# Kernel optimization log

Measured on AMD Instinct MI355X. Metric: run time of the kernel, lower is better.

## Reference

```python
import itertools
import jax, jax.numpy as jnp
import numpy as np


def _lin(x, w, b):
    # LogitsInference with logic_hidden_dim=[] is a single Linear (logits).
    return jnp.einsum('...i,oi->...o', x, w) + b


def _permute_cat(x, order):
    # Permutation(order): concat over all permutations of the `order` variable axes.
    if order <= 1:
        return x
    nd = x.ndim  # [B, n x order, C]
    return jnp.concatenate(
        [jnp.transpose(x, (0,) + p + (nd - 1,))
         for p in itertools.permutations(range(1, order + 1))], axis=-1)


def _expand(x, i, n):
    # Expander(i-1): insert a new object axis at position i (after existing var axes).
    x = jnp.expand_dims(x, axis=i)
    shape = list(x.shape)
    shape[i] = n
    return jnp.broadcast_to(x, tuple(shape))


def _reduce(x, order_in):
    # Reducer(order_in, exclude_self=True): mask entries with repeated indices among
    # the order_in variable axes, then take exists(max)/forall(min) over the last
    # variable axis and interleave channels -> 2*C.
    n = x.shape[1]
    if order_in >= 2:
        idx = [jnp.arange(n).reshape((1,) * k + (n,) + (1,) * (order_in - k - 1))
               for k in range(order_in)]
        mask = jnp.ones((n,) * order_in, dtype=bool)
        for a in range(order_in):
            for b in range(a + 1, order_in):
                mask = mask & (idx[a] != idx[b])
        mask = mask[None, ..., None]  # [1, n x order_in, 1]
        inp0 = jnp.where(mask, x, jnp.zeros((), x.dtype))
        inp1 = jnp.where(mask, x, jnp.ones((), x.dtype))
    else:
        inp0 = inp1 = x
    exists = jnp.max(inp0, axis=-2)
    forall = jnp.min(inp1, axis=-2)
    out = jnp.stack([exists, forall], axis=-1)  # interleave like torch stack+view
    return out.reshape(out.shape[:-2] + (out.shape[-2] * 2,))


def _bmask(act, bit, ndim):
    return act[:, bit].astype(jnp.float32).reshape((-1,) + (1,) * (ndim - 1))


def _logic_layer(x0, x1, x2, x3,
                 w_op0, b_op0, w_red0, b_red0,
                 w_exp1, b_exp1, w_op1, b_op1, w_red1, b_red1,
                 w_exp2, b_exp2, w_op2, b_op2, w_red2, b_red2,
                 w_exp3, b_exp3, w_op3, b_op3, act):
    n = x1.shape[1]
    # Per-batch-item bit masks replace index_select/index_copy_ (same math:
    # selected rows get the branch output, others contribute zero to the sum).
    # order 0: bits 0 (direct), 1 (reduce from order 1)
    s0 = (_bmask(act, 0, 2) * _lin(x0, w_op0, b_op0)
          + _bmask(act, 1, 2) * _lin(_reduce(x1, 1), w_red0, b_red0))
    o0 = jnp.where(jnp.any(act[:, 0:2] == 1), jax.nn.sigmoid(s0), jnp.zeros_like(s0))
    # order 1: bits 2 (expand from 0), 3 (direct), 4 (reduce from 2)
    s1 = (_bmask(act, 2, 3) * _lin(_expand(x0, 1, n), w_exp1, b_exp1)
          + _bmask(act, 3, 3) * _lin(x1, w_op1, b_op1)
          + _bmask(act, 4, 3) * _lin(_reduce(x2, 2), w_red1, b_red1))
    o1 = jnp.where(jnp.any(act[:, 2:5] == 1), jax.nn.sigmoid(s1), jnp.zeros_like(s1))
    # order 2: bits 5 (expand), 6 (direct), 7 (reduce)
    s2 = (_bmask(act, 5, 4) * _lin(_permute_cat(_expand(x1, 2, n), 2), w_exp2, b_exp2)
          + _bmask(act, 6, 4) * _lin(_permute_cat(x2, 2), w_op2, b_op2)
          + _bmask(act, 7, 4) * _lin(_permute_cat(_reduce(x3, 3), 2), w_red2, b_red2))
    o2 = jnp.where(jnp.any(act[:, 5:8] == 1), jax.nn.sigmoid(s2), jnp.zeros_like(s2))
    # order 3 (= max_order): bits 8 (expand), 9 (direct)
    s3 = (_bmask(act, 8, 5) * _lin(_permute_cat(_expand(x2, 3, n), 3), w_exp3, b_exp3)
          + _bmask(act, 9, 5) * _lin(_permute_cat(x3, 3), w_op3, b_op3))
    o3 = jnp.where(jnp.any(act[:, 8:10] == 1), jax.nn.sigmoid(s3), jnp.zeros_like(s3))
    return (o0, o1, o2, o3)


def setup_inputs() -> dict:
    key = jax.random.key(0)
    B, n, C, O = 8, 32, 64, 64
    ks = list(jax.random.split(key, 32))
    ki = iter(ks)
    d = {}
    d['x0'] = jax.random.normal(next(ki), (B, C), jnp.float32)
    d['x1'] = jax.random.normal(next(ki), (B, n, C), jnp.float32)
    d['x2'] = jax.random.normal(next(ki), (B, n, n, C), jnp.float32)
    d['x3'] = jax.random.normal(next(ki), (B, n, n, n, C), jnp.float32)
    in_dims = {'w_op0': C, 'w_red0': 2 * C,
               'w_exp1': C, 'w_op1': C, 'w_red1': 2 * C,
               'w_exp2': 2 * C, 'w_op2': 2 * C, 'w_red2': 4 * C,
               'w_exp3': 6 * C, 'w_op3': 6 * C}
    for name, ind in in_dims.items():
        d[name] = jax.random.normal(next(ki), (O, ind), jnp.float32) * 0.05
        d['b' + name[1:]] = jnp.zeros((O,), jnp.float32)
    d['act'] = jax.random.randint(next(ki), (B, 10), 0, 2, dtype=jnp.int32)
    return d


def reference(x0, x1, x2, x3,
              w_op0, b_op0, w_red0, b_red0,
              w_exp1, b_exp1, w_op1, b_op1, w_red1, b_red1,
              w_exp2, b_exp2, w_op2, b_op2, w_red2, b_red2,
              w_exp3, b_exp3, w_op3, b_op3, act):
    return _logic_layer(x0, x1, x2, x3,
                        w_op0, b_op0, w_red0, b_red0,
                        w_exp1, b_exp1, w_op1, b_op1, w_red1, b_red1,
                        w_exp2, b_exp2, w_op2, b_op2, w_red2, b_red2,
                        w_exp3, b_exp3, w_op3, b_op3, act)
```

## Files before the change

### kernel.cpp

```cpp
#include <hip/hip_runtime.h>
#include <hip/hip_bf16.h>
#include <math.h>

#define NB 8
#define NN 32
#define NC 64
#define NO 64

#define WS_G    0
#define WS_MF   16
#define WS_R1   128
#define WS_R2   2048
#define WS_X1B  36864
#define WS_X2B  45056
#define WS_R3B  307200
#define WS_BB   831488
#define WS_BB2  832000
#define WS_WC   832512
#define WS_WC2  1029120
#define WS_R2B  1160192
#define WS_WC1  1176576
#define WS_X0B  1242112
#define WS_BB1  1242368

typedef short bf16x8 __attribute__((ext_vector_type(8)));
typedef unsigned short u16x4 __attribute__((ext_vector_type(4)));
typedef unsigned short u16x8 __attribute__((ext_vector_type(8)));
typedef float f32x4 __attribute__((ext_vector_type(4)));

__device__ __forceinline__ float sigmoidf_(float s) {
    return 1.0f / (1.0f + expf(-s));
}

__device__ __forceinline__ unsigned short f2b(float x) {
    union { __hip_bfloat16 h; unsigned short u; } v;
    v.h = __float2bfloat16(x);
    return v.u;
}

__global__ void prep_all(const float* __restrict__ x0,
                         const float* __restrict__ we3, const float* __restrict__ wo3,
                         const float* __restrict__ we2, const float* __restrict__ wo2,
                         const float* __restrict__ wr2,
                         const float* __restrict__ we1, const float* __restrict__ wo1,
                         const float* __restrict__ wr1,
                         const float* __restrict__ be1, const float* __restrict__ bo1,
                         const float* __restrict__ br1,
                         const float* __restrict__ be2, const float* __restrict__ bo2,
                         const float* __restrict__ br2,
                         const float* __restrict__ be3, const float* __restrict__ bo3,
                         const int* __restrict__ act, float* __restrict__ ws) {
    int bb = blockIdx.x, t = threadIdx.x;
    if (bb < 1536) {
        int tid = bb * 256 + t;
        unsigned short* wc = (unsigned short*)(ws + WS_WC);
        int i8 = tid & 7;
        int lane = (tid >> 3) & 63;
        int rest = tid >> 9;
        int kk = rest % 24;
        int ntb = rest / 24;
        int nt = ntb & 3, b = ntb >> 2;
        int o = nt * 16 + (lane & 15);
        int kloc = kk * 32 + ((lane >> 4) << 3) + i8;
        bool m8 = act[b * 10 + 8] == 1;
        bool m9 = act[b * 10 + 9] == 1;
        float val;
        if (kloc < 384) val = m8 ? we3[o * 384 + kloc] : 0.0f;
        else            val = m9 ? wo3[o * 384 + kloc - 384] : 0.0f;
        wc[tid] = f2b(val);
    } else if (bb < 2560) {
        int tid = (bb - 1536) * 256 + t;
        unsigned short* wc2 = (unsigned short*)(ws + WS_WC2);
        int i8 = tid & 7;
        int lane = (tid >> 3) & 63;
        int rest = tid >> 9;
        int kk = rest & 15;
        int ntb = rest >> 4;
        int nt = ntb & 3, b = ntb >> 2;
        int o = nt * 16 + (lane & 15);
        int kloc = kk * 32 + ((lane >> 4) << 3) + i8;
        float val;
        if (kloc < 128)      val = (act[b * 10 + 5] == 1) ? we2[o * 128 + kloc] : 0.0f;
        else if (kloc < 256) val = (act[b * 10 + 6] == 1) ? wo2[o * 128 + kloc - 128] : 0.0f;
        else                 val = (act[b * 10 + 7] == 1) ? wr2[o * 256 + kloc - 256] : 0.0f;
        wc2[tid] = f2b(val);
    } else if (bb < 3072) {
        int tid = (bb - 2560) * 256 + t;
        unsigned short* wc1 = (unsigned short*)(ws + WS_WC1);
        int i8 = tid & 7;
        int lane = (tid >> 3) & 63;
        int rest = tid >> 9;
        int kk = rest & 7;
        int ntb = rest >> 3;
        int nt = ntb & 3, b = ntb >> 2;
        int o = nt * 16 + (lane & 15);
        int kloc = kk * 32 + ((lane >> 4) << 3) + i8;
        float val;
        if (kloc < 64)       val = (act[b * 10 + 2] == 1) ? we1[o * 64 + kloc] : 0.0f;
        else if (kloc < 128) val = (act[b * 10 + 3] == 1) ? wo1[o * 64 + kloc - 64] : 0.0f;
        else                 val = (act[b * 10 + 4] == 1) ? wr1[o * 128 + kloc - 128] : 0.0f;
        wc1[tid] = f2b(val);
    } else {
        int t512 = (bb - 3072) * 256 + t;
        int b = t512 >> 6, o = t512 & 63;
        float m2 = (act[b * 10 + 2] == 1) ? 1.0f : 0.0f;
        float m3 = (act[b * 10 + 3] == 1) ? 1.0f : 0.0f;
        float m4 = (act[b * 10 + 4] == 1) ? 1.0f : 0.0f;
        float m5 = (act[b * 10 + 5] == 1) ? 1.0f : 0.0f;
        float m6 = (act[b * 10 + 6] == 1) ? 1.0f : 0.0f;
        float m7 = (act[b * 10 + 7] == 1) ? 1.0f : 0.0f;
        float m8 = (act[b * 10 + 8] == 1) ? 1.0f : 0.0f;
        float m9 = (act[b * 10 + 9] == 1) ? 1.0f : 0.0f;
        ws[WS_BB1 + t512] = m2 * be1[o] + m3 * bo1[o] + m4 * br1[o];
        ws[WS_BB2 + t512] = m5 * be2[o] + m6 * bo2[o] + m7 * br2[o];
        ws[WS_BB  + t512] = m8 * be3[o] + m9 * bo3[o];
        unsigned short* x0b = (unsigned short*)(ws + WS_X0B);
        x0b[t512] = f2b(x0[t512]);
        if (t512 < 80) ws[WS_MF + t512] = (act[t512] == 1) ? 1.0f : 0.0f;
        if (t512 < 4) {
            const int lo[4] = {0, 2, 5, 8};
            const int hi[4] = {2, 5, 8, 10};
            int any = 0;
            for (int bx = 0; bx < NB; ++bx)
                for (int bit = lo[t512]; bit < hi[t512]; ++bit)
                    any |= (act[bx * 10 + bit] == 1);
            ws[WS_G + t512] = any ? 1.0f : 0.0f;
        }
    }
}

__global__ __launch_bounds__(64) void red1(const float* __restrict__ x1, float* __restrict__ ws) {
    int b = blockIdx.x, c = threadIdx.x;
    unsigned short* x1b = (unsigned short*)(ws + WS_X1B);
    float mx = -INFINITY, mn = INFINITY;
    for (int k = 0; k < NN; ++k) {
        float v = x1[(b * NN + k) * NC + c];
        x1b[(b * NN + k) * NC + c] = f2b(v);
        mx = fmaxf(mx, v); mn = fminf(mn, v);
    }
    ws[WS_R1 + b * 2 * NC + 2 * c]     = mx;
    ws[WS_R1 + b * 2 * NC + 2 * c + 1] = mn;
}

__global__ __launch_bounds__(64) void red2(const float* __restrict__ x2, float* __restrict__ ws) {
    int blk = blockIdx.x; int i = blk % NN, b = blk / NN; int c = threadIdx.x;
    unsigned short* x2b = (unsigned short*)(ws + WS_X2B);
    unsigned short* r2b = (unsigned short*)(ws + WS_R2B);
    float mx = -INFINITY, mn = INFINITY;
    for (int jj = 0; jj < NN; ++jj) {
        float v = x2[((b * NN + i) * NN + jj) * NC + c];
        x2b[((b * NN + i) * NN + jj) * NC + c] = f2b(v);
        mx = fmaxf(mx, (jj == i) ? 0.0f : v);
        mn = fminf(mn, (jj == i) ? 1.0f : v);
    }
    ws[WS_R2 + (b * NN + i) * 2 * NC + 2 * c]     = mx;
    ws[WS_R2 + (b * NN + i) * 2 * NC + 2 * c + 1] = mn;
    unsigned int packed = (unsigned int)f2b(mx) | ((unsigned int)f2b(mn) << 16);
    *(unsigned int*)(r2b + (b * NN + i) * 128 + 2 * c) = packed;
}

__global__ __launch_bounds__(64) void red3(const float* __restrict__ x3, float* __restrict__ ws) {
    int blk = blockIdx.x;
    int j = blk & 31, i = (blk >> 5) & 31, b = blk >> 10;
    int t = threadIdx.x;
    int kg = t >> 4, c4 = (t & 15) << 2;
    const float* base = x3 + (size_t)(((b * 32 + i) * 32 + j) * 32) * 64;
    float mx[4] = {-INFINITY, -INFINITY, -INFINITY, -INFINITY};
    float mn[4] = {INFINITY, INFINITY, INFINITY, INFINITY};
    bool alldiag = (i == j);
    #pragma unroll
    for (int it = 0; it < 8; ++it) {
        int k = it * 4 + kg;
        f32x4 v = *(const f32x4*)(base + k * 64 + c4);
        bool bad = alldiag || (k == i) || (k == j);
        #pragma unroll
        for (int q = 0; q < 4; ++q) {
            mx[q] = fmaxf(mx[q], bad ? 0.0f : v[q]);
            mn[q] = fminf(mn[q], bad ? 1.0f : v[q]);
        }
    }
    #pragma unroll
    for (int off = 16; off < 64; off <<= 1) {
        #pragma unroll
        for (int q = 0; q < 4; ++q) {
            mx[q] = fmaxf(mx[q], __shfl_xor(mx[q], off, 64));
            mn[q] = fminf(mn[q], __shfl_xor(mn[q], off, 64));
        }
    }
    if (t < 16) {
        u16x8 h;
        #pragma unroll
        for (int q = 0; q < 4; ++q) { h[2 * q] = f2b(mx[q]); h[2 * q + 1] = f2b(mn[q]); }
        unsigned short* r3b = (unsigned short*)(ws + WS_R3B);
        *(u16x8*)(r3b + (size_t)((b * 32 + i) * 32 + j) * 128 + t * 8) = h;
    }
}

__global__ __launch_bounds__(64) void out0k(
        const float* __restrict__ x0,
        const float* __restrict__ w_op0, const float* __restrict__ b_op0,
        const float* __restrict__ w_red0, const float* __restrict__ b_red0,
        const float* __restrict__ ws, float* __restrict__ out) {
    int b = blockIdx.x, o = threadIdx.x;
    float g  = ws[WS_G + 0];
    float m0 = ws[WS_MF + b * 10 + 0], m1 = ws[WS_MF + b * 10 + 1];
    float d0 = b_op0[o];
    for (int c = 0; c < NC; ++c) d0 += w_op0[o * NC + c] * x0[b * NC + c];
    float d1 = b_red0[o];
    for (int c = 0; c < 2 * NC; ++c) d1 += w_red0[o * 2 * NC + c] * ws[WS_R1 + b * 2 * NC + c];
    float s = m0 * d0 + m1 * d1;
    out[b * NO + o] = (g != 0.0f) ? sigmoidf_(s) : 0.0f;
}

__global__ __launch_bounds__(256) void out1k_mfma(
        const float* __restrict__ ws_f, float* __restrict__ out) {
    __shared__ unsigned short A[32 * 256];
    int b = blockIdx.x;
    int t = threadIdx.x;
    int lane = t & 63, nt = t >> 6;
    const unsigned short* x0b = (const unsigned short*)(ws_f + WS_X0B);
    const unsigned short* x1b = (const unsigned short*)(ws_f + WS_X1B);
    const unsigned short* r2b = (const unsigned short*)(ws_f + WS_R2B);
    const unsigned short* wc1 = (const unsigned short*)(ws_f + WS_WC1);
    char* Ab = (char*)A;
    int r = t >> 3, c8 = (t & 7) << 3;
    int sw = (r & 7) << 4;
    {
        bf16x8 v0 = *(const bf16x8*)(x0b + b * 64 + c8);
        bf16x8 v1 = *(const bf16x8*)(x1b + (b * 32 + r) * 64 + c8);
        bf16x8 v2 = *(const bf16x8*)(r2b + (b * 32 + r) * 128 + c8);
        bf16x8 v3 = *(const bf16x8*)(r2b + (b * 32 + r) * 128 + 64 + c8);
        *(bf16x8*)(Ab + ((r * 512 + (0 * 64 + c8) * 2) ^ sw)) = v0;
        *(bf16x8*)(Ab + ((r * 512 + (1 * 64 + c8) * 2) ^ sw)) = v1;
        *(bf16x8*)(Ab + ((r * 512 + (2 * 64 + c8) * 2) ^ sw)) = v2;
        *(bf16x8*)(Ab + ((r * 512 + (3 * 64 + c8) * 2) ^ sw)) = v3;
    }
    __syncthreads();
    f32x4 acc0 = {0.f, 0.f, 0.f, 0.f};
    f32x4 acc1 = {0.f, 0.f, 0.f, 0.f};
    const unsigned short* wblk = wc1 + (size_t)((b * 4 + nt) * 8) * 512 + lane * 8;
    int arow0 = lane & 15, arow1 = 16 + arow0;
    int kgrp2 = ((lane >> 4) << 3) * 2;
    int sw0 = (arow0 & 7) << 4;
    #pragma unroll
    for (int kk = 0; kk < 8; ++kk) {
        int kloc2 = kk * 64 + kgrp2;
        bf16x8 a0 = *(const bf16x8*)(Ab + ((arow0 * 512 + kloc2) ^ sw0));
        bf16x8 a1 = *(const bf16x8*)(Ab + ((arow1 * 512 + kloc2) ^ sw0));
        bf16x8 bw = *(const bf16x8*)(wblk + kk * 512);
        acc0 = __builtin_amdgcn_mfma_f32_16x16x32_bf16(a0, bw, acc0, 0, 0, 0);
        acc1 = __builtin_amdgcn_mfma_f32_16x16x32_bf16(a1, bw, acc1, 0, 0, 0);
    }
    float g1 = ws_f[WS_G + 1];
    int o = nt * 16 + (lane & 15);
    float bias = ws_f[WS_BB1 + b * 64 + o];
    int rgrp = (lane >> 4) << 2;
    float* obase = out + b * 2048;
    #pragma unroll
    for (int rr = 0; rr < 4; ++rr) {
        float s0 = acc0[rr] + bias;
        float s1 = acc1[rr] + bias;
        obase[(rgrp + rr) * 64 + o]      = (g1 != 0.0f) ? sigmoidf_(s0) : 0.0f;
        obase[(16 + rgrp + rr) * 64 + o] = (g1 != 0.0f) ? sigmoidf_(s1) : 0.0f;
    }
}

__global__ __launch_bounds__(256) void out2k_mfma(
        const float* __restrict__ ws_f, float* __restrict__ out) {
    __shared__ unsigned short A[32 * 512];
    int blk = blockIdx.x;
    int i = blk & 31, b = blk >> 5;
    int t = threadIdx.x;
    int lane = t & 63, nt = t >> 6;
    const unsigned short* x1b = (const unsigned short*)(ws_f + WS_X1B);
    const unsigned short* x2b = (const unsigned short*)(ws_f + WS_X2B);
    const unsigned short* r3b = (const unsigned short*)(ws_f + WS_R3B);
    const unsigned short* wc2 = (const unsigned short*)(ws_f + WS_WC2);
    char* Ab = (char*)A;
    int r8 = t >> 3, c8 = (t & 7) << 3;
    {
        bf16x8 v0 = *(const bf16x8*)(x1b + (b * 32 + i) * 64 + c8);
        bf16x8 v1 = *(const bf16x8*)(x1b + b * 2048 + r8 * 64 + c8);
        bf16x8 v2 = *(const bf16x8*)(x2b + ((b * 32 + i) * 32) * 64 + r8 * 64 + c8);
        bf16x8 v3 = *(const bf16x8*)(x2b + (b * 1024 + i) * 64 + r8 * 2048 + c8);
        int sw = (r8 & 7) << 4;
        *(bf16x8*)(Ab + ((r8 * 1024 + (0 * 64 + c8) * 2) ^ sw)) = v0;
        *(bf16x8*)(Ab + ((r8 * 1024 + (1 * 64 + c8) * 2) ^ sw)) = v1;
        *(bf16x8*)(Ab + ((r8 * 1024 + (2 * 64 + c8) * 2) ^ sw)) = v2;
        *(bf16x8*)(Ab + ((r8 * 1024 + (3 * 64 + c8) * 2) ^ sw)) = v3;
    }
    int r16 = t >> 4, c16 = (t & 15) << 3;
    #pragma unroll
    for (int p = 0; p < 2; ++p) {
        int jr = p * 16 + r16;
        bf16x8 v4 = *(const bf16x8*)(r3b + ((b * 32 + i) * 32 + jr) * 128 + c16);
        bf16x8 v5 = *(const bf16x8*)(r3b + ((b * 32 + jr) * 32 + i) * 128 + c16);
        int sw = (jr & 7) << 4;
        *(bf16x8*)(Ab + ((jr * 1024 + (256 + c16) * 2) ^ sw)) = v4;
        *(bf16x8*)(Ab + ((jr * 1024 + (384 + c16) * 2) ^ sw)) = v5;
    }
    __syncthreads();
    f32x4 acc0 = {0.f, 0.f, 0.f, 0.f};
    f32x4 acc1 = {0.f, 0.f, 0.f, 0.f};
    const unsigned short* wblk = wc2 + (size_t)((b * 4 + nt) * 16) * 512 + lane * 8;
    int arow0 = lane & 15, arow1 = 16 + arow0;
    int kgrp2 = ((lane >> 4) << 3) * 2;
    int sw0 = (arow0 & 7) << 4;
    #pragma unroll
    for (int kk = 0; kk < 16; ++kk) {
        int kloc2 = kk * 64 + kgrp2;
        bf16x8 a0 = *(const bf16x8*)(Ab + ((arow0 * 1024 + kloc2) ^ sw0));
        bf16x8 a1 = *(const bf16x8*)(Ab + ((arow1 * 1024 + kloc2) ^ sw0));
        bf16x8 bf = *(const bf16x8*)(wblk + kk * 512);
        acc0 = __builtin_amdgcn_mfma_f32_16x16x32_bf16(a0, bf, acc0, 0, 0, 0);
        acc1 = __builtin_amdgcn_mfma_f32_16x16x32_bf16(a1, bf, acc1, 0, 0, 0);
    }
    float g2 = ws_f[WS_G + 2];
    int o = nt * 16 + (lane & 15);
    float bias = ws_f[WS_BB2 + b * 64 + o];
    int rgrp = (lane >> 4) << 2;
    float* obase = out + (size_t)((b * 32 + i) * 32) * 64;
    #pragma unroll
    for (int r = 0; r < 4; ++r) {
        float s0 = acc0[r] + bias;
        float s1 = acc1[r] + bias;
        obase[(rgrp + r) * 64 + o]      = (g2 != 0.0f) ? sigmoidf_(s0) : 0.0f;
        obase[(16 + rgrp + r) * 64 + o] = (g2 != 0.0f) ? sigmoidf_(s1) : 0.0f;
    }
}

__global__ __launch_bounds__(256) void out3k_mfma(
        const float* __restrict__ x3, const float* __restrict__ ws_f,
        float* __restrict__ out) {
    __shared__ unsigned short A[16 * 768];
    int blk = blockIdx.x;
    int j = blk & 31, i = (blk >> 5) & 31, b = blk >> 10;
    int t = threadIdx.x;
    int lane = t & 63, wv = t >> 6;
    const unsigned short* x2b = (const unsigned short*)(ws_f + WS_X2B);
    const unsigned short* wc = (const unsigned short*)(ws_f + WS_WC);
    char* Ab = (char*)A;

    size_t cb[6]; int cs[6];
    cb[0] = ((b * 32 + i) * 32 + j) * 64; cs[0] = 0;
    cb[1] = ((b * 32 + i) * 32) * 64;     cs[1] = 64;
    cb[2] = ((b * 32 + j) * 32 + i) * 64; cs[2] = 0;
    cb[3] = (b * 1024 + i) * 64;          cs[3] = 2048;
    cb[4] = ((b * 32 + j) * 32) * 64;     cs[4] = 64;
    cb[5] = (b * 1024 + j) * 64;          cs[5] = 2048;
    const float* xb[6]; int xs[6];
    xb[0] = x3 + (size_t)(((b * 32 + i) * 32 + j) * 32) * 64; xs[0] = 64;
    xb[1] = x3 + (size_t)(((b * 32 + i) * 32) * 32 + j) * 64; xs[1] = 2048;
    xb[2] = x3 + (size_t)(((b * 32 + j) * 32 + i) * 32) * 64; xs[2] = 64;
    xb[3] = x3 + (size_t)((b * 1024 + i) * 32 + j) * 64;      xs[3] = 65536;
    xb[4] = x3 + (size_t)(((b * 32 + j) * 32) * 32 + i) * 64; xs[4] = 2048;
    xb[5] = x3 + (size_t)(b * 32768 + j * 32 + i) * 64;       xs[5] = 65536;

    auto stage = [&](int h) {
        int r = t >> 3;
        int row = r & 15;
        int k = h * 16 + row;
        int cset = (r >> 4) * 3;
        int c8 = (t & 7) << 3;
        int sw = (row & 7) << 4;
        #pragma unroll
        for (int cc = 0; cc < 3; ++cc) {
            int ch = cset + cc;
            bf16x8 v = *(const bf16x8*)(x2b + cb[ch] + (size_t)k * cs[ch] + c8);
            *(bf16x8*)(Ab + ((row * 1536 + (ch * 64 + c8) * 2) ^ sw)) = v;
        }
        int row2 = t >> 4;
        int k2 = h * 16 + row2;
        int c4 = (t & 15) << 2;
        int sw2 = (row2 & 7) << 4;
        #pragma unroll
        for (int ch = 0; ch < 6; ++ch) {
            f32x4 v = *(const f32x4*)(xb[ch] + (size_t)k2 * xs[ch] + c4);
            u16x4 hh = { f2b(v[0]), f2b(v[1]), f2b(v[2]), f2b(v[3]) };
            *(u16x4*)(Ab + ((row2 * 1536 + ((6 + ch) * 64 + c4) * 2) ^ sw2)) = hh;
        }
    };

    const unsigned short* wblk = wc + (size_t)((b * 4 + wv) * 24) * 512 + lane * 8;
    int arow = lane & 15;
    int kgrp2 = ((lane >> 4) << 3) * 2;
    int sw0 = (arow & 7) << 4;
    f32x4 acc0 = {0.f, 0.f, 0.f, 0.f};
    f32x4 acc1 = {0.f, 0.f, 0.f, 0.f};

    stage(0);
    __syncthreads();
    #pragma unroll 4
    for (int kk = 0; kk < 24; ++kk) {
        int kloc2 = kk * 64 + kgrp2;
        bf16x8 a0 = *(const bf16x8*)(Ab + ((arow * 1536 + kloc2) ^ sw0));
        bf16x8 bf = *(const bf16x8*)(wblk + kk * 512);
        acc0 = __builtin_amdgcn_mfma_f32_16x16x32_bf16(a0, bf, acc0, 0, 0, 0);
    }
    __syncthreads();
    stage(1);
    __syncthreads();
    #pragma unroll 4
    for (int kk = 0; kk < 24; ++kk) {
        int kloc2 = kk * 64 + kgrp2;
        bf16x8 a1 = *(const bf16x8*)(Ab + ((arow * 1536 + kloc2) ^ sw0));
        bf16x8 bf = *(const bf16x8*)(wblk + kk * 512);
        acc1 = __builtin_amdgcn_mfma_f32_16x16x32_bf16(a1, bf, acc1, 0, 0, 0);
    }

    float g3 = ws_f[WS_G + 3];
    int o = wv * 16 + (lane & 15);
    float bias = ws_f[WS_BB + b * 64 + o];
    int rgrp = (lane >> 4) << 2;
    float* obase = out + (size_t)(((b * 32 + i) * 32 + j) * 32) * 64;
    #pragma unroll
    for (int r = 0; r < 4; ++r) {
        float s0 = acc0[r] + bias;
        float s1 = acc1[r] + bias;
        obase[(rgrp + r) * 64 + o]      = (g3 != 0.0f) ? sigmoidf_(s0) : 0.0f;
        obase[(16 + rgrp + r) * 64 + o] = (g3 != 0.0f) ? sigmoidf_(s1) : 0.0f;
    }
}

extern "C" void kernel_launch(void* const* d_in, const int* in_sizes, int n_in,
                              void* d_out, int out_size, void* d_ws, size_t ws_size,
                              hipStream_t stream) {
    const float* x0 = (const float*)d_in[0];
    const float* x1 = (const float*)d_in[1];
    const float* x2 = (const float*)d_in[2];
    const float* x3 = (const float*)d_in[3];
    const float* w_op0 = (const float*)d_in[4];   const float* b_op0 = (const float*)d_in[5];
    const float* w_red0 = (const float*)d_in[6];  const float* b_red0 = (const float*)d_in[7];
    const float* w_exp1 = (const float*)d_in[8];  const float* b_exp1 = (const float*)d_in[9];
    const float* w_op1 = (const float*)d_in[10];  const float* b_op1 = (const float*)d_in[11];
    const float* w_red1 = (const float*)d_in[12]; const float* b_red1 = (const float*)d_in[13];
    const float* w_exp2 = (const float*)d_in[14]; const float* b_exp2 = (const float*)d_in[15];
    const float* w_op2 = (const float*)d_in[16];  const float* b_op2 = (const float*)d_in[17];
    const float* w_red2 = (const float*)d_in[18]; const float* b_red2 = (const float*)d_in[19];
    const float* w_exp3 = (const float*)d_in[20]; const float* b_exp3 = (const float*)d_in[21];
    const float* w_op3 = (const float*)d_in[22];  const float* b_op3 = (const float*)d_in[23];
    const int* act = (const int*)d_in[24];

    float* ws = (float*)d_ws;
    float* out = (float*)d_out;
    float* out0 = out;
    float* out1 = out + 512;
    float* out2 = out + 16896;
    float* out3 = out + 541184;

    prep_all<<<3074, 256, 0, stream>>>(x0, w_exp3, w_op3, w_exp2, w_op2, w_red2,
                                       w_exp1, w_op1, w_red1,
                                       b_exp1, b_op1, b_red1,
                                       b_exp2, b_op2, b_red2,
                                       b_exp3, b_op3, act, ws);
    red1<<<NB, 64, 0, stream>>>(x1, ws);
    red2<<<NB * NN, 64, 0, stream>>>(x2, ws);
    red3<<<NB * NN * NN, 64, 0, stream>>>(x3, ws);
    out0k<<<NB, 64, 0, stream>>>(x0, w_op0, b_op0, w_red0, b_red0, ws, out0);
    out1k_mfma<<<NB, 256, 0, stream>>>(ws, out1);
    out2k_mfma<<<NB * NN, 256, 0, stream>>>(ws, out2);
    out3k_mfma<<<NB * NN * NN, 256, 0, stream>>>(x3, ws, out3);
}
```

Baseline: 258.8 us.

## Fuse x3 reduction into symmetric-pair out3 kernel and merge small launches

Each out3 block now handles an unordered pair (i,j) and loads the 12 staged channel slices once. Both the (i,j) and (j,i) outputs are computed from the same A tile by permuting weight blocks, and the red3 masked max/min reduction is taken from shared memory. The x1/x2 reductions fold into prep_all, and out0/out1 merge into one launch. This removes the separate full pass over x3 and several launches, at the cost of a larger shared tile and more register pressure. out2 now runs after out3, which reads the r3b reductions out3 writes.

Result: faster. 228.4 us (-11.8%).

```diff
diff --git a/kernel.cpp b/kernel.cpp
--- a/kernel.cpp
+++ b/kernel.cpp
@@ -25,7 +25,6 @@
 
 typedef short bf16x8 __attribute__((ext_vector_type(8)));
 typedef unsigned short u16x4 __attribute__((ext_vector_type(4)));
-typedef unsigned short u16x8 __attribute__((ext_vector_type(8)));
 typedef float f32x4 __attribute__((ext_vector_type(4)));
 
 __device__ __forceinline__ float sigmoidf_(float s) {
@@ -38,18 +37,26 @@
     return v.u;
 }
 
-__global__ void prep_all(const float* __restrict__ x0,
-                         const float* __restrict__ we3, const float* __restrict__ wo3,
-                         const float* __restrict__ we2, const float* __restrict__ wo2,
-                         const float* __restrict__ wr2,
-                         const float* __restrict__ we1, const float* __restrict__ wo1,
-                         const float* __restrict__ wr1,
-                         const float* __restrict__ be1, const float* __restrict__ bo1,
-                         const float* __restrict__ br1,
-                         const float* __restrict__ be2, const float* __restrict__ bo2,
-                         const float* __restrict__ br2,
-                         const float* __restrict__ be3, const float* __restrict__ bo3,
-                         const int* __restrict__ act, float* __restrict__ ws) {
+__device__ __forceinline__ float b2f(unsigned short u) {
+    union { unsigned int u; float f; } v; v.u = ((unsigned int)u) << 16;
+    return v.f;
+}
+
+__global__ __launch_bounds__(256) void prep_all(
+        const float* __restrict__ x0, const float* __restrict__ x1,
+        const float* __restrict__ x2,
+        const float* __restrict__ we3, const float* __restrict__ wo3,
+        const float* __restrict__ we2, const float* __restrict__ wo2,
+        const float* __restrict__ wr2,
+        const float* __restrict__ we1, const float* __restrict__ wo1,
+        const float* __restrict__ wr1,
+        const float* __restrict__ be1, const float* __restrict__ bo1,
+        const float* __restrict__ br1,
+        const float* __restrict__ be2, const float* __restrict__ bo2,
+        const float* __restrict__ br2,
+        const float* __restrict__ be3, const float* __restrict__ bo3,
+        const int* __restrict__ act, float* __restrict__ ws) {
+    __shared__ float pmx[4][64], pmn[4][64];
     int bb = blockIdx.x, t = threadIdx.x;
     if (bb < 1536) {
         int tid = bb * 256 + t;
@@ -100,7 +107,7 @@
         else if (kloc < 128) val = (act[b * 10 + 3] == 1) ? wo1[o * 64 + kloc - 64] : 0.0f;
         else                 val = (act[b * 10 + 4] == 1) ? wr1[o * 128 + kloc - 128] : 0.0f;
         wc1[tid] = f2b(val);
-    } else {
+    } else if (bb < 3074) {
         int t512 = (bb - 3072) * 256 + t;
         int b = t512 >> 6, o = t512 & 63;
         float m2 = (act[b * 10 + 2] == 1) ? 1.0f : 0.0f;
@@ -126,97 +133,186 @@
                     any |= (act[bx * 10 + bit] == 1);
             ws[WS_G + t512] = any ? 1.0f : 0.0f;
         }
-    }
-}
-
-__global__ __launch_bounds__(64) void red1(const float* __restrict__ x1, float* __restrict__ ws) {
-    int b = blockIdx.x, c = threadIdx.x;
-    unsigned short* x1b = (unsigned short*)(ws + WS_X1B);
-    float mx = -INFINITY, mn = INFINITY;
-    for (int k = 0; k < NN; ++k) {
-        float v = x1[(b * NN + k) * NC + c];
-        x1b[(b * NN + k) * NC + c] = f2b(v);
-        mx = fmaxf(mx, v); mn = fminf(mn, v);
-    }
-    ws[WS_R1 + b * 2 * NC + 2 * c]     = mx;
-    ws[WS_R1 + b * 2 * NC + 2 * c + 1] = mn;
-}
-
-__global__ __launch_bounds__(64) void red2(const float* __restrict__ x2, float* __restrict__ ws) {
-    int blk = blockIdx.x; int i = blk % NN, b = blk / NN; int c = threadIdx.x;
-    unsigned short* x2b = (unsigned short*)(ws + WS_X2B);
-    unsigned short* r2b = (unsigned short*)(ws + WS_R2B);
-    float mx = -INFINITY, mn = INFINITY;
-    for (int jj = 0; jj < NN; ++jj) {
-        float v = x2[((b * NN + i) * NN + jj) * NC + c];
-        x2b[((b * NN + i) * NN + jj) * NC + c] = f2b(v);
-        mx = fmaxf(mx, (jj == i) ? 0.0f : v);
-        mn = fminf(mn, (jj == i) ? 1.0f : v);
-    }
-    ws[WS_R2 + (b * NN + i) * 2 * NC + 2 * c]     = mx;
-    ws[WS_R2 + (b * NN + i) * 2 * NC + 2 * c + 1] = mn;
-    unsigned int packed = (unsigned int)f2b(mx) | ((unsigned int)f2b(mn) << 16);
-    *(unsigned int*)(r2b + (b * NN + i) * 128 + 2 * c) = packed;
-}
-
-__global__ __launch_bounds__(64) void red3(const float* __restrict__ x3, float* __restrict__ ws) {
+    } else if (bb < 3082) {
+        if (t < 64) {
+            int b = bb - 3074, c = t;
+            unsigned short* x1b = (unsigned short*)(ws + WS_X1B);
+            float mx = -INFINITY, mn = INFINITY;
+            for (int k = 0; k < NN; ++k) {
+                float v = x1[(b * NN + k) * NC + c];
+                x1b[(b * NN + k) * NC + c] = f2b(v);
+                mx = fmaxf(mx, v); mn = fminf(mn, v);
+            }
+            ws[WS_R1 + b * 2 * NC + 2 * c]     = mx;
+            ws[WS_R1 + b * 2 * NC + 2 * c + 1] = mn;
+        }
+    } else {
+        int idx = bb - 3082;
+        int i = idx & 31, b = idx >> 5;
+        int w = t >> 6, c = t & 63;
+        unsigned short* x2b = (unsigned short*)(ws + WS_X2B);
+        float mx = -INFINITY, mn = INFINITY;
+        #pragma unroll
+        for (int q = 0; q < 8; ++q) {
+            int jj = w * 8 + q;
+            float v = x2[((b * NN + i) * NN + jj) * NC + c];
+            x2b[((b * NN + i) * NN + jj) * NC + c] = f2b(v);
+            mx = fmaxf(mx, (jj == i) ? 0.0f : v);
+            mn = fminf(mn, (jj == i) ? 1.0f : v);
+        }
+        pmx[w][c] = mx; pmn[w][c] = mn;
+        __syncthreads();
+        if (t < 64) {
+            mx = fmaxf(fmaxf(pmx[0][c], pmx[1][c]), fmaxf(pmx[2][c], pmx[3][c]));
+            mn = fminf(fminf(pmn[0][c], pmn[1][c]), fminf(pmn[2][c], pmn[3][c]));
+            unsigned short* r2b = (unsigned short*)(ws + WS_R2B);
+            unsigned int packed = (unsigned int)f2b(mx) | ((unsigned int)f2b(mn) << 16);
+            *(unsigned int*)(r2b + (b * NN + i) * 128 + 2 * c) = packed;
+        }
+    }
+}
+
+__global__ __launch_bounds__(256) void out3k_pair(
+        const float* __restrict__ x3, const float* __restrict__ ws_f,
+        float* __restrict__ out) {
+    __shared__ unsigned short A[32 * 768];
     int blk = blockIdx.x;
-    int j = blk & 31, i = (blk >> 5) & 31, b = blk >> 10;
+    int b = blk / 528, pi = blk - b * 528;
+    float fsq = sqrtf(4225.0f - 8.0f * (float)pi);
+    int i = (int)((65.0f - fsq) * 0.5f);
+    while (i > 0 && (i * (65 - i)) / 2 > pi) --i;
+    while (((i + 1) * (64 - i)) / 2 <= pi) ++i;
+    int j = i + (pi - (i * (65 - i)) / 2);
+
     int t = threadIdx.x;
-    int kg = t >> 4, c4 = (t & 15) << 2;
-    const float* base = x3 + (size_t)(((b * 32 + i) * 32 + j) * 32) * 64;
-    float mx[4] = {-INFINITY, -INFINITY, -INFINITY, -INFINITY};
-    float mn[4] = {INFINITY, INFINITY, INFINITY, INFINITY};
-    bool alldiag = (i == j);
-    #pragma unroll
-    for (int it = 0; it < 8; ++it) {
-        int k = it * 4 + kg;
-        f32x4 v = *(const f32x4*)(base + k * 64 + c4);
-        bool bad = alldiag || (k == i) || (k == j);
+    int lane = t & 63, wv = t >> 6;
+    const unsigned short* x2b = (const unsigned short*)(ws_f + WS_X2B);
+    const unsigned short* wc = (const unsigned short*)(ws_f + WS_WC);
+    char* Ab = (char*)A;
+
+    {
+        int r8 = t >> 3, c8 = (t & 7) << 3;
+        size_t cb[6]; int cs[6];
+        cb[0] = ((b * 32 + i) * 32 + j) * 64; cs[0] = 0;
+        cb[1] = ((b * 32 + i) * 32) * 64;     cs[1] = 64;
+        cb[2] = ((b * 32 + j) * 32 + i) * 64; cs[2] = 0;
+        cb[3] = (b * 1024 + i) * 64;          cs[3] = 2048;
+        cb[4] = ((b * 32 + j) * 32) * 64;     cs[4] = 64;
+        cb[5] = (b * 1024 + j) * 64;          cs[5] = 2048;
+        int sw = (r8 & 7) << 4;
         #pragma unroll
-        for (int q = 0; q < 4; ++q) {
-            mx[q] = fmaxf(mx[q], bad ? 0.0f : v[q]);
-            mn[q] = fminf(mn[q], bad ? 1.0f : v[q]);
-        }
-    }
-    #pragma unroll
-    for (int off = 16; off < 64; off <<= 1) {
+        for (int ch = 0; ch < 6; ++ch) {
+            bf16x8 v = *(const bf16x8*)(x2b + cb[ch] + (size_t)r8 * cs[ch] + c8);
+            *(bf16x8*)(Ab + ((r8 * 1536 + (ch * 64 + c8) * 2) ^ sw)) = v;
+        }
+        int r16 = t >> 4, c4 = (t & 15) << 2;
+        const float* xb[6]; int xs[6];
+        xb[0] = x3 + (size_t)(((b * 32 + i) * 32 + j) * 32) * 64; xs[0] = 64;
+        xb[1] = x3 + (size_t)(((b * 32 + i) * 32) * 32 + j) * 64; xs[1] = 2048;
+        xb[2] = x3 + (size_t)(((b * 32 + j) * 32 + i) * 32) * 64; xs[2] = 64;
+        xb[3] = x3 + (size_t)((b * 1024 + i) * 32 + j) * 64;      xs[3] = 65536;
+        xb[4] = x3 + (size_t)(((b * 32 + j) * 32) * 32 + i) * 64; xs[4] = 2048;
+        xb[5] = x3 + (size_t)(b * 32768 + j * 32 + i) * 64;       xs[5] = 65536;
         #pragma unroll
-        for (int q = 0; q < 4; ++q) {
-            mx[q] = fmaxf(mx[q], __shfl_xor(mx[q], off, 64));
-            mn[q] = fminf(mn[q], __shfl_xor(mn[q], off, 64));
-        }
-    }
-    if (t < 16) {
-        u16x8 h;
+        for (int ch = 0; ch < 6; ++ch) {
+            #pragma unroll
+            for (int p = 0; p < 2; ++p) {
+                int k = p * 16 + r16;
+                f32x4 v = *(const f32x4*)(xb[ch] + (size_t)k * xs[ch] + c4);
+                u16x4 hh = { f2b(v[0]), f2b(v[1]), f2b(v[2]), f2b(v[3]) };
+                *(u16x4*)(Ab + ((k * 1536 + ((6 + ch) * 64 + c4) * 2) ^ ((k & 7) << 4))) = hh;
+            }
+        }
+    }
+    __syncthreads();
+
+    f32x4 acc00 = {0.f,0.f,0.f,0.f}, acc01 = {0.f,0.f,0.f,0.f};
+    f32x4 acc10 = {0.f,0.f,0.f,0.f}, acc11 = {0.f,0.f,0.f,0.f};
+    const unsigned short* wblk = wc + (size_t)((b * 4 + wv) * 24) * 512 + lane * 8;
+    int arow = lane & 15;
+    int kgrp2 = ((lane >> 4) << 3) * 2;
+    int sw0 = (arow & 7) << 4;
+    const int P1[12] = {2, 4, 0, 5, 1, 3, 8, 10, 6, 11, 7, 9};
+    #pragma unroll
+    for (int c = 0; c < 12; ++c) {
         #pragma unroll
-        for (int q = 0; q < 4; ++q) { h[2 * q] = f2b(mx[q]); h[2 * q + 1] = f2b(mn[q]); }
-        unsigned short* r3b = (unsigned short*)(ws + WS_R3B);
-        *(u16x8*)(r3b + (size_t)((b * 32 + i) * 32 + j) * 128 + t * 8) = h;
-    }
-}
-
-__global__ __launch_bounds__(64) void out0k(
+        for (int s = 0; s < 2; ++s) {
+            int colb = c * 128 + s * 64 + kgrp2;
+            bf16x8 a0 = *(const bf16x8*)(Ab + ((arow * 1536 + colb) ^ sw0));
+            bf16x8 a1 = *(const bf16x8*)(Ab + (((arow + 16) * 1536 + colb) ^ sw0));
+            bf16x8 w0 = *(const bf16x8*)(wblk + (2 * c + s) * 512);
+            bf16x8 w1 = *(const bf16x8*)(wblk + (2 * P1[c] + s) * 512);
+            acc00 = __builtin_amdgcn_mfma_f32_16x16x32_bf16(a0, w0, acc00, 0, 0, 0);
+            acc01 = __builtin_amdgcn_mfma_f32_16x16x32_bf16(a1, w0, acc01, 0, 0, 0);
+            acc10 = __builtin_amdgcn_mfma_f32_16x16x32_bf16(a0, w1, acc10, 0, 0, 0);
+            acc11 = __builtin_amdgcn_mfma_f32_16x16x32_bf16(a1, w1, acc11, 0, 0, 0);
+        }
+    }
+
+    if (wv == 0 || (wv == 1 && i != j)) {
+        int c = lane;
+        int colbase = (wv == 0) ? 384 : 512;
+        float mx = 0.0f, mn = 1.0f;
+        if (i != j) {
+            for (int k = 0; k < 32; ++k) {
+                if (k == i || k == j) continue;
+                int addr = (k * 1536 + (colbase + c) * 2) ^ ((k & 7) << 4);
+                float v = b2f(*(const unsigned short*)(Ab + addr));
+                mx = fmaxf(mx, v); mn = fminf(mn, v);
+            }
+        }
+        unsigned short* r3b = (unsigned short*)(ws_f + WS_R3B);
+        int slot = (wv == 0) ? ((b * 32 + i) * 32 + j) : ((b * 32 + j) * 32 + i);
+        unsigned int packed = (unsigned int)f2b(mx) | ((unsigned int)f2b(mn) << 16);
+        *(unsigned int*)(r3b + (size_t)slot * 128 + 2 * c) = packed;
+    }
+
+    float g3 = ws_f[WS_G + 3];
+    int o = wv * 16 + (lane & 15);
+    float bias = ws_f[WS_BB + b * 64 + o];
+    int rgrp = (lane >> 4) << 2;
+    float* ob0 = out + (size_t)(((b * 32 + i) * 32 + j) * 32) * 64;
+    float* ob1 = out + (size_t)(((b * 32 + j) * 32 + i) * 32) * 64;
+    #pragma unroll
+    for (int r = 0; r < 4; ++r) {
+        float s0 = acc00[r] + bias;
+        float s1 = acc01[r] + bias;
+        ob0[(rgrp + r) * 64 + o]      = (g3 != 0.0f) ? sigmoidf_(s0) : 0.0f;
+        ob0[(16 + rgrp + r) * 64 + o] = (g3 != 0.0f) ? sigmoidf_(s1) : 0.0f;
+    }
+    if (i != j) {
+        #pragma unroll
+        for (int r = 0; r < 4; ++r) {
+            float s0 = acc10[r] + bias;
+            float s1 = acc11[r] + bias;
+            ob1[(rgrp + r) * 64 + o]      = (g3 != 0.0f) ? sigmoidf_(s0) : 0.0f;
+            ob1[(16 + rgrp + r) * 64 + o] = (g3 != 0.0f) ? sigmoidf_(s1) : 0.0f;
+        }
+    }
+}
+
+__global__ __launch_bounds__(256) void out01(
         const float* __restrict__ x0,
         const float* __restrict__ w_op0, const float* __restrict__ b_op0,
         const float* __restrict__ w_red0, const float* __restrict__ b_red0,
-        const float* __restrict__ ws, float* __restrict__ out) {
-    int b = blockIdx.x, o = threadIdx.x;
-    float g  = ws[WS_G + 0];
-    float m0 = ws[WS_MF + b * 10 + 0], m1 = ws[WS_MF + b * 10 + 1];
-    float d0 = b_op0[o];
-    for (int c = 0; c < NC; ++c) d0 += w_op0[o * NC + c] * x0[b * NC + c];
-    float d1 = b_red0[o];
-    for (int c = 0; c < 2 * NC; ++c) d1 += w_red0[o * 2 * NC + c] * ws[WS_R1 + b * 2 * NC + c];
-    float s = m0 * d0 + m1 * d1;
-    out[b * NO + o] = (g != 0.0f) ? sigmoidf_(s) : 0.0f;
-}
-
-__global__ __launch_bounds__(256) void out1k_mfma(
-        const float* __restrict__ ws_f, float* __restrict__ out) {
+        const float* __restrict__ ws_f, float* __restrict__ out0,
+        float* __restrict__ out1) {
     __shared__ unsigned short A[32 * 256];
-    int b = blockIdx.x;
-    int t = threadIdx.x;
+    int bb = blockIdx.x, t = threadIdx.x;
+    if (bb < 8) {
+        if (t >= 64) return;
+        int b = bb, o = t;
+        float g  = ws_f[WS_G + 0];
+        float m0 = ws_f[WS_MF + b * 10 + 0], m1 = ws_f[WS_MF + b * 10 + 1];
+        float d0 = b_op0[o];
+        for (int c = 0; c < NC; ++c) d0 += w_op0[o * NC + c] * x0[b * NC + c];
+        float d1 = b_red0[o];
+        for (int c = 0; c < 2 * NC; ++c) d1 += w_red0[o * 2 * NC + c] * ws_f[WS_R1 + b * 2 * NC + c];
+        float s = m0 * d0 + m1 * d1;
+        out0[b * NO + o] = (g != 0.0f) ? sigmoidf_(s) : 0.0f;
+        return;
+    }
+    int b = bb - 8;
     int lane = t & 63, nt = t >> 6;
     const unsigned short* x0b = (const unsigned short*)(ws_f + WS_X0B);
     const unsigned short* x1b = (const unsigned short*)(ws_f + WS_X1B);
@@ -236,8 +332,8 @@
         *(bf16x8*)(Ab + ((r * 512 + (3 * 64 + c8) * 2) ^ sw)) = v3;
     }
     __syncthreads();
-    f32x4 acc0 = {0.f, 0.f, 0.f, 0.f};
-    f32x4 acc1 = {0.f, 0.f, 0.f, 0.f};
+    f32x4 acc0 = {0.f,0.f,0.f,0.f};
+    f32x4 acc1 = {0.f,0.f,0.f,0.f};
     const unsigned short* wblk = wc1 + (size_t)((b * 4 + nt) * 8) * 512 + lane * 8;
     int arow0 = lane & 15, arow1 = 16 + arow0;
     int kgrp2 = ((lane >> 4) << 3) * 2;
@@ -255,7 +351,7 @@
     int o = nt * 16 + (lane & 15);
     float bias = ws_f[WS_BB1 + b * 64 + o];
     int rgrp = (lane >> 4) << 2;
-    float* obase = out + b * 2048;
+    float* obase = out1 + b * 2048;
     #pragma unroll
     for (int rr = 0; rr < 4; ++rr) {
         float s0 = acc0[rr] + bias;
@@ -300,8 +396,8 @@
         *(bf16x8*)(Ab + ((jr * 1024 + (384 + c16) * 2) ^ sw)) = v5;
     }
     __syncthreads();
-    f32x4 acc0 = {0.f, 0.f, 0.f, 0.f};
-    f32x4 acc1 = {0.f, 0.f, 0.f, 0.f};
+    f32x4 acc0 = {0.f,0.f,0.f,0.f};
+    f32x4 acc1 = {0.f,0.f,0.f,0.f};
     const unsigned short* wblk = wc2 + (size_t)((b * 4 + nt) * 16) * 512 + lane * 8;
     int arow0 = lane & 15, arow1 = 16 + arow0;
     int kgrp2 = ((lane >> 4) << 3) * 2;
@@ -326,99 +422,6 @@
         float s1 = acc1[r] + bias;
         obase[(rgrp + r) * 64 + o]      = (g2 != 0.0f) ? sigmoidf_(s0) : 0.0f;
         obase[(16 + rgrp + r) * 64 + o] = (g2 != 0.0f) ? sigmoidf_(s1) : 0.0f;
-    }
-}
-
-__global__ __launch_bounds__(256) void out3k_mfma(
-        const float* __restrict__ x3, const float* __restrict__ ws_f,
-        float* __restrict__ out) {
-    __shared__ unsigned short A[16 * 768];
-    int blk = blockIdx.x;
-    int j = blk & 31, i = (blk >> 5) & 31, b = blk >> 10;
-    int t = threadIdx.x;
-    int lane = t & 63, wv = t >> 6;
-    const unsigned short* x2b = (const unsigned short*)(ws_f + WS_X2B);
-    const unsigned short* wc = (const unsigned short*)(ws_f + WS_WC);
-    char* Ab = (char*)A;
-
-    size_t cb[6]; int cs[6];
-    cb[0] = ((b * 32 + i) * 32 + j) * 64; cs[0] = 0;
-    cb[1] = ((b * 32 + i) * 32) * 64;     cs[1] = 64;
-    cb[2] = ((b * 32 + j) * 32 + i) * 64; cs[2] = 0;
-    cb[3] = (b * 1024 + i) * 64;          cs[3] = 2048;
-    cb[4] = ((b * 32 + j) * 32) * 64;     cs[4] = 64;
-    cb[5] = (b * 1024 + j) * 64;          cs[5] = 2048;
-    const float* xb[6]; int xs[6];
-    xb[0] = x3 + (size_t)(((b * 32 + i) * 32 + j) * 32) * 64; xs[0] = 64;
-    xb[1] = x3 + (size_t)(((b * 32 + i) * 32) * 32 + j) * 64; xs[1] = 2048;
-    xb[2] = x3 + (size_t)(((b * 32 + j) * 32 + i) * 32) * 64; xs[2] = 64;
-    xb[3] = x3 + (size_t)((b * 1024 + i) * 32 + j) * 64;      xs[3] = 65536;
-    xb[4] = x3 + (size_t)(((b * 32 + j) * 32) * 32 + i) * 64; xs[4] = 2048;
-    xb[5] = x3 + (size_t)(b * 32768 + j * 32 + i) * 64;       xs[5] = 65536;
-
-    auto stage = [&](int h) {
-        int r = t >> 3;
-        int row = r & 15;
-        int k = h * 16 + row;
-        int cset = (r >> 4) * 3;
-        int c8 = (t & 7) << 3;
-        int sw = (row & 7) << 4;
-        #pragma unroll
-        for (int cc = 0; cc < 3; ++cc) {
-            int ch = cset + cc;
-            bf16x8 v = *(const bf16x8*)(x2b + cb[ch] + (size_t)k * cs[ch] + c8);
-            *(bf16x8*)(Ab + ((row * 1536 + (ch * 64 + c8) * 2) ^ sw)) = v;
-        }
-        int row2 = t >> 4;
-        int k2 = h * 16 + row2;
-        int c4 = (t & 15) << 2;
-        int sw2 = (row2 & 7) << 4;
-        #pragma unroll
-        for (int ch = 0; ch < 6; ++ch) {
-            f32x4 v = *(const f32x4*)(xb[ch] + (size_t)k2 * xs[ch] + c4);
-            u16x4 hh = { f2b(v[0]), f2b(v[1]), f2b(v[2]), f2b(v[3]) };
-            *(u16x4*)(Ab + ((row2 * 1536 + ((6 + ch) * 64 + c4) * 2) ^ sw2)) = hh;
-        }
-    };
-
-    const unsigned short* wblk = wc + (size_t)((b * 4 + wv) * 24) * 512 + lane * 8;
-    int arow = lane & 15;
-    int kgrp2 = ((lane >> 4) << 3) * 2;
-    int sw0 = (arow & 7) << 4;
-    f32x4 acc0 = {0.f, 0.f, 0.f, 0.f};
-    f32x4 acc1 = {0.f, 0.f, 0.f, 0.f};
-
-    stage(0);
-    __syncthreads();
-    #pragma unroll 4
-    for (int kk = 0; kk < 24; ++kk) {
-        int kloc2 = kk * 64 + kgrp2;
-        bf16x8 a0 = *(const bf16x8*)(Ab + ((arow * 1536 + kloc2) ^ sw0));
-        bf16x8 bf = *(const bf16x8*)(wblk + kk * 512);
-        acc0 = __builtin_amdgcn_mfma_f32_16x16x32_bf16(a0, bf, acc0, 0, 0, 0);
-    }
-    __syncthreads();
-    stage(1);
-    __syncthreads();
-    #pragma unroll 4
-    for (int kk = 0; kk < 24; ++kk) {
-        int kloc2 = kk * 64 + kgrp2;
-        bf16x8 a1 = *(const bf16x8*)(Ab + ((arow * 1536 + kloc2) ^ sw0));
-        bf16x8 bf = *(const bf16x8*)(wblk + kk * 512);
-        acc1 = __builtin_amdgcn_mfma_f32_16x16x32_bf16(a1, bf, acc1, 0, 0, 0);
-    }
-
-    float g3 = ws_f[WS_G + 3];
-    int o = wv * 16 + (lane & 15);
-    float bias = ws_f[WS_BB + b * 64 + o];
-    int rgrp = (lane >> 4) << 2;
-    float* obase = out + (size_t)(((b * 32 + i) * 32 + j) * 32) * 64;
-    #pragma unroll
-    for (int r = 0; r < 4; ++r) {
-        float s0 = acc0[r] + bias;
-        float s1 = acc1[r] + bias;
-        obase[(rgrp + r) * 64 + o]      = (g3 != 0.0f) ? sigmoidf_(s0) : 0.0f;
-        obase[(16 + rgrp + r) * 64 + o] = (g3 != 0.0f) ? sigmoidf_(s1) : 0.0f;
     }
 }
 
@@ -448,16 +451,13 @@
     float* out2 = out + 16896;
     float* out3 = out + 541184;
 
-    prep_all<<<3074, 256, 0, stream>>>(x0, w_exp3, w_op3, w_exp2, w_op2, w_red2,
+    prep_all<<<3338, 256, 0, stream>>>(x0, x1, x2,
+                                       w_exp3, w_op3, w_exp2, w_op2, w_red2,
                                        w_exp1, w_op1, w_red1,
                                        b_exp1, b_op1, b_red1,
                                        b_exp2, b_op2, b_red2,
                                        b_exp3, b_op3, act, ws);
-    red1<<<NB, 64, 0, stream>>>(x1, ws);
-    red2<<<NB * NN, 64, 0, stream>>>(x2, ws);
-    red3<<<NB * NN * NN, 64, 0, stream>>>(x3, ws);
-    out0k<<<NB, 64, 0, stream>>>(x0, w_op0, b_op0, w_red0, b_red0, ws, out0);
-    out1k_mfma<<<NB, 256, 0, stream>>>(ws, out1);
+    out3k_pair<<<NB * 528, 256, 0, stream>>>(x3, ws, out3);
+    out01<<<16, 256, 0, stream>>>(x0, w_op0, b_op0, w_red0, b_red0, ws, out0, out1);
     out2k_mfma<<<NB * NN, 256, 0, stream>>>(ws, out2);
-    out3k_mfma<<<NB * NN * NN, 256, 0, stream>>>(x3, ws, out3);
-}
+}
```
